# Kernel tuning notes

Hardware: AMD Instinct MI355X
Metric: run time of the kernel (lower is better)

## Reference

```python
import jax, jax.numpy as jnp
import numpy as np

N_NODES = 100000
N_EDGES = 1600000
N_GRAPHS = 64
EMB_DIM = 64
DIMS = [6, 16, 32, 64, EMB_DIM]


def setup_inputs() -> dict:
    key = jax.random.key(0)
    ks = jax.random.split(key, 16)
    feat = jax.random.normal(ks[0], (N_NODES, DIMS[0]), dtype=jnp.float32)
    src = jax.random.randint(ks[1], (N_EDGES,), 0, N_NODES)
    dst = jax.random.randint(ks[2], (N_EDGES,), 0, N_NODES)
    graph_ids = jnp.sort(jax.random.randint(ks[3], (N_NODES,), 0, N_GRAPHS))
    inp = {"feat": feat, "src": src, "dst": dst, "graph_ids": graph_ids}
    # fc_neigh weights for each SAGEConv (gcn aggregator has no fc_self), Xavier-ish init
    for i in range(4):
        din, dout = DIMS[i], DIMS[i + 1]
        scale = 1.0 / np.sqrt(din)
        inp[f"W{i+1}"] = jax.random.uniform(ks[4 + 2 * i], (din, dout), jnp.float32, -scale, scale)
        inp[f"b{i+1}"] = jnp.zeros((dout,), jnp.float32)
    return inp


def _sage_gcn(feat, src, dst, deg, W, b):
    # DGL SAGEConv aggregator_type='gcn':
    # h_neigh = (sum_{u in N(v)} h_u + h_v) / (in_deg(v) + 1); out = h_neigh @ W + b
    neigh = jax.ops.segment_sum(feat[src], dst, num_segments=N_NODES)  # [N, din]
    h = (neigh + feat) / (deg[:, None] + 1.0)
    return h @ W + b


def reference(feat, src, dst, graph_ids, W1, b1, W2, b2, W3, b3, W4, b4):
    deg = jax.ops.segment_sum(jnp.ones((N_EDGES,), feat.dtype), dst, num_segments=N_NODES)
    h = feat
    for W, b in ((W1, b1), (W2, b2), (W3, b3), (W4, b4)):
        h = jax.nn.relu(_sage_gcn(h, src, dst, deg, W, b))
    # dgl.mean_nodes: per-graph mean over nodes
    sums = jax.ops.segment_sum(h, graph_ids, num_segments=N_GRAPHS)          # [G, emb]
    cnts = jax.ops.segment_sum(jnp.ones((N_NODES,), h.dtype), graph_ids, num_segments=N_GRAPHS)
    return sums / jnp.maximum(cnts, 1.0)[:, None]
```

## Files before the change

kernel.cpp:

```cpp
#include <hip/hip_runtime.h>
#include <hip/hip_bf16.h>
#include <hip/hip_fp16.h>

#define N_NODES 100000
#define N_EDGES 1600000
#define N_GRAPHS 64

#define NB_BKT 256
#define NPBKT 391
#define EPB 2048
#define NBLK_BIN ((N_EDGES + EPB - 1) / EPB)


__device__ __forceinline__ __half2 u2h(unsigned int u) {
    return __builtin_bit_cast(__half2, u);
}
__device__ __forceinline__ float2 u2f2(unsigned int u) {
    return __half22float2(u2h(u));
}
__device__ __forceinline__ unsigned int packh2(float a, float b) {
    return __builtin_bit_cast(unsigned int, __float22half2_rn(make_float2(a, b)));
}


__global__ __launch_bounds__(256) void bin_count(const int* __restrict__ dst,
                                                 int* __restrict__ cntmat, int E) {
    __shared__ int cnt[NB_BKT];
    int t = threadIdx.x;
    int e0 = blockIdx.x * EPB;
    cnt[t] = 0;
    __syncthreads();
#pragma unroll
    for (int k = 0; k < 8; ++k) {
        int e = e0 + k * 256 + t;
        if (e < E) {
            unsigned d = (unsigned)dst[e];
            atomicAdd(&cnt[d / (unsigned)NPBKT], 1);
        }
    }
    __syncthreads();
    cntmat[(size_t)blockIdx.x * NB_BKT + t] = cnt[t];
}

__global__ __launch_bounds__(256) void bin_scan(int* __restrict__ cntmat,
                                                int* __restrict__ gcnt, int nblk) {
    __shared__ int s[256];
    int b = blockIdx.x, t = threadIdx.x;
    int running = 0;
    for (int c0 = 0; c0 < nblk; c0 += 256) {
        int idx = c0 + t;
        int v = (idx < nblk) ? cntmat[(size_t)idx * NB_BKT + b] : 0;
        s[t] = v;
        __syncthreads();
        for (int o = 1; o < 256; o <<= 1) {
            int a = (t >= o) ? s[t - o] : 0;
            __syncthreads();
            s[t] += a;
            __syncthreads();
        }
        if (idx < nblk) cntmat[(size_t)idx * NB_BKT + b] = running + s[t] - v;
        running += s[255];
        __syncthreads();
    }
    if (t == 0) gcnt[b] = running;
}

__global__ __launch_bounds__(256) void bin_write(const int* __restrict__ dst,
                                                 const int* __restrict__ src,
                                                 const int* __restrict__ cntmat,
                                                 const int* __restrict__ gcnt,
                                                 uint2* __restrict__ rec, int E) {
    __shared__ int cnt[NB_BKT];
    __shared__ int lbase[NB_BKT];
    __shared__ int gofs[NB_BKT];
    __shared__ uint2 stage[EPB];
    int t = threadIdx.x;
    int e0 = blockIdx.x * EPB;
    int g = gcnt[t];
    lbase[t] = g;
    __syncthreads();
    for (int o = 1; o < 256; o <<= 1) {
        int a = (t >= o) ? lbase[t - o] : 0;
        __syncthreads();
        lbase[t] += a;
        __syncthreads();
    }
    gofs[t] = (lbase[t] - g) + cntmat[(size_t)blockIdx.x * NB_BKT + t];
    cnt[t] = 0;
    __syncthreads();
    int myb[8], mypos[8];
    unsigned myd[8], mys[8];
#pragma unroll
    for (int k = 0; k < 8; ++k) {
        int e = e0 + k * 256 + t;
        if (e < E) {
            unsigned d = (unsigned)dst[e];
            int b = (int)(d / (unsigned)NPBKT);
            myd[k] = d;
            mys[k] = (unsigned)src[e];
            myb[k] = b;
            mypos[k] = atomicAdd(&cnt[b], 1);
        } else {
            myb[k] = -1;
        }
    }
    __syncthreads();
    int c = cnt[t];
    lbase[t] = c;
    __syncthreads();
    for (int o = 1; o < 256; o <<= 1) {
        int a = (t >= o) ? lbase[t - o] : 0;
        __syncthreads();
        lbase[t] += a;
        __syncthreads();
    }
    lbase[t] = lbase[t] - c;
    __syncthreads();
#pragma unroll
    for (int k = 0; k < 8; ++k)
        if (myb[k] >= 0) stage[lbase[myb[k]] + mypos[k]] = make_uint2(myd[k], mys[k]);
    __syncthreads();
    int total = min(EPB, E - e0);
    for (int i = t; i < total; i += 256) {
        int lo = 0, hi = NB_BKT - 1;
        while (lo < hi) {
            int m = (lo + hi + 1) >> 1;
            if (lbase[m] <= i) lo = m; else hi = m - 1;
        }
        rec[(size_t)gofs[lo] + (i - lbase[lo])] = stage[i];
    }
}

__global__ __launch_bounds__(256) void fill_bucket(const uint2* __restrict__ rec,
                                                   const int* __restrict__ gcnt,
                                                   int* __restrict__ rp,
                                                   int* __restrict__ col, int n) {
    __shared__ int sdeg[512];
    __shared__ int lcur[512];
    __shared__ int sg[256];
    __shared__ int lcol[8192];
    int p = blockIdx.x, t = threadIdx.x;
    int nbase = p * NPBKT;
    int nn = min(NPBKT, n - nbase);
    int g = gcnt[t];
    sg[t] = g;
    __syncthreads();
    for (int o = 1; o < 256; o <<= 1) {
        int a = (t >= o) ? sg[t - o] : 0;
        __syncthreads();
        sg[t] += a;
        __syncthreads();
    }
    int ex = sg[t] - g;
    __syncthreads();
    sg[t] = ex;
    __syncthreads();
    int cbase = sg[p];
    int cnt = gcnt[p];
    sdeg[t] = 0;
    sdeg[t + 256] = 0;
    __syncthreads();
    const uint2* r = rec + cbase;
    for (int i = t; i < cnt; i += 256) atomicAdd(&sdeg[r[i].x - (unsigned)nbase], 1);
    __syncthreads();
    int c0 = sdeg[t], c1 = sdeg[t + 256];
    for (int o = 1; o < 512; o <<= 1) {
        int a = (t >= o) ? sdeg[t - o] : 0;
        int b = (t + 256 >= o) ? sdeg[t + 256 - o] : 0;
        __syncthreads();
        sdeg[t] += a;
        sdeg[t + 256] += b;
        __syncthreads();
    }
    int ex0 = sdeg[t] - c0, ex1 = sdeg[t + 256] - c1;
    lcur[t] = ex0;
    lcur[t + 256] = ex1;
    if (t < nn) rp[nbase + t] = cbase + ex0;
    if (t + 256 < nn) rp[nbase + t + 256] = cbase + ex1;
    if (p == NB_BKT - 1 && t == 0) rp[n] = cbase + cnt;
    __syncthreads();
    for (int i = t; i < cnt; i += 256) {
        uint2 e = r[i];
        int slot = atomicAdd(&lcur[e.x - (unsigned)nbase], 1);
        lcol[slot] = (int)e.y;
    }
    __syncthreads();
    for (int i = t; i < cnt; i += 256) col[cbase + i] = lcol[i];
}


__global__ __launch_bounds__(256) void sage_layer1(const float* __restrict__ feat,
                                                   const int* __restrict__ rp,
                                                   const int* __restrict__ col,
                                                   const float* __restrict__ W,
                                                   const float* __restrict__ bias,
                                                   unsigned int* __restrict__ hout, int n) {
    __shared__ float sW[6 * 16];
    __shared__ float sB[16];
    int tid = threadIdx.x;
    if (tid < 96) sW[tid] = W[tid];
    if (tid < 16) sB[tid] = bias[tid];
    __syncthreads();
    int v = blockIdx.x * 256 + tid;
    if (v >= n) return;
    int r0 = rp[v], r1 = rp[v + 1];
    float acc[6] = {0.f, 0.f, 0.f, 0.f, 0.f, 0.f};
    const float2* f2 = reinterpret_cast<const float2*>(feat);
    int j = r0;
    for (; j + 4 <= r1; j += 4) {
        int u0 = col[j], u1 = col[j + 1], u2 = col[j + 2], u3 = col[j + 3];
        float2 a0 = f2[u0 * 3 + 0], b0 = f2[u0 * 3 + 1], c0 = f2[u0 * 3 + 2];
        float2 a1 = f2[u1 * 3 + 0], b1 = f2[u1 * 3 + 1], c1 = f2[u1 * 3 + 2];
        float2 a2 = f2[u2 * 3 + 0], b2 = f2[u2 * 3 + 1], c2 = f2[u2 * 3 + 2];
        float2 a3 = f2[u3 * 3 + 0], b3 = f2[u3 * 3 + 1], c3 = f2[u3 * 3 + 2];
        acc[0] += (a0.x + a1.x) + (a2.x + a3.x);
        acc[1] += (a0.y + a1.y) + (a2.y + a3.y);
        acc[2] += (b0.x + b1.x) + (b2.x + b3.x);
        acc[3] += (b0.y + b1.y) + (b2.y + b3.y);
        acc[4] += (c0.x + c1.x) + (c2.x + c3.x);
        acc[5] += (c0.y + c1.y) + (c2.y + c3.y);
    }
    for (; j < r1; ++j) {
        int u = col[j];
        float2 a = f2[u * 3 + 0], b = f2[u * 3 + 1], c = f2[u * 3 + 2];
        acc[0] += a.x; acc[1] += a.y;
        acc[2] += b.x; acc[3] += b.y;
        acc[4] += c.x; acc[5] += c.y;
    }
    {
        float2 a = f2[v * 3 + 0], b = f2[v * 3 + 1], c = f2[v * 3 + 2];
        acc[0] += a.x; acc[1] += a.y;
        acc[2] += b.x; acc[3] += b.y;
        acc[4] += c.x; acc[5] += c.y;
    }
    float inv = 1.0f / (float)(r1 - r0 + 1);
#pragma unroll
    for (int k = 0; k < 6; ++k) acc[k] *= inv;
    float outv[16];
#pragma unroll
    for (int o = 0; o < 16; ++o) outv[o] = sB[o];
#pragma unroll
    for (int k = 0; k < 6; ++k) {
#pragma unroll
        for (int o = 0; o < 16; ++o) outv[o] += acc[k] * sW[k * 16 + o];
    }
    unsigned int w[8];
#pragma unroll
    for (int o = 0; o < 16; o += 2)
        w[o / 2] = packh2(fmaxf(outv[o], 0.f), fmaxf(outv[o + 1], 0.f));
    uint4* op = reinterpret_cast<uint4*>(hout + v * 8);
    op[0] = make_uint4(w[0], w[1], w[2], w[3]);
    op[1] = make_uint4(w[4], w[5], w[6], w[7]);
}


template <int DIN, int DOUT>
__global__ __launch_bounds__(256) void sage_f16(const uint4* __restrict__ hin,
                                                const int* __restrict__ rp,
                                                const int* __restrict__ col,
                                                const float* __restrict__ W,
                                                const float* __restrict__ bias,
                                                unsigned int* __restrict__ hout, int n) {
    constexpr int WPN = DIN / 8;
    constexpr int NPB = 256 / WPN;
    constexpr int OPT = DOUT / WPN;
    __shared__ float sW[DIN * DOUT];
    __shared__ float sB[DOUT];
    __shared__ float sH[NPB][DIN + 1];

    int tid = threadIdx.x;
    for (int i = tid; i < DIN * DOUT; i += 256) sW[i] = W[i];
    if (tid < DOUT) sB[tid] = bias[tid];

    int sub = tid / WPN;
    int t = tid % WPN;
    int v = blockIdx.x * NPB + sub;

    if (v < n) {
        int r0 = rp[v], r1 = rp[v + 1];
        const __half2 z = __float2half2_rn(0.f);
        __half2 acc[4][4];
#pragma unroll
        for (int s = 0; s < 4; ++s)
#pragma unroll
            for (int q = 0; q < 4; ++q) acc[s][q] = z;
        int j = r0;
        for (; j + 8 <= r1; j += 8) {
            uint4 w[8];
#pragma unroll
            for (int k = 0; k < 8; ++k) w[k] = hin[col[j + k] * WPN + t];
#pragma unroll
            for (int k = 0; k < 8; ++k) {
                __half2* a = acc[k & 3];
                a[0] = __hadd2(a[0], u2h(w[k].x));
                a[1] = __hadd2(a[1], u2h(w[k].y));
                a[2] = __hadd2(a[2], u2h(w[k].z));
                a[3] = __hadd2(a[3], u2h(w[k].w));
            }
        }
        for (; j + 4 <= r1; j += 4) {
            uint4 w[4];
#pragma unroll
            for (int k = 0; k < 4; ++k) w[k] = hin[col[j + k] * WPN + t];
#pragma unroll
            for (int k = 0; k < 4; ++k) {
                __half2* a = acc[k];
                a[0] = __hadd2(a[0], u2h(w[k].x));
                a[1] = __hadd2(a[1], u2h(w[k].y));
                a[2] = __hadd2(a[2], u2h(w[k].z));
                a[3] = __hadd2(a[3], u2h(w[k].w));
            }
        }
        for (; j < r1; ++j) {
            uint4 w = hin[col[j] * WPN + t];
            acc[0][0] = __hadd2(acc[0][0], u2h(w.x));
            acc[0][1] = __hadd2(acc[0][1], u2h(w.y));
            acc[0][2] = __hadd2(acc[0][2], u2h(w.z));
            acc[0][3] = __hadd2(acc[0][3], u2h(w.w));
        }
#pragma unroll
        for (int q = 0; q < 4; ++q)
            acc[0][q] = __hadd2(__hadd2(acc[0][q], acc[1][q]),
                                __hadd2(acc[2][q], acc[3][q]));
        uint4 ws = hin[v * WPN + t];
        unsigned swd[4] = {ws.x, ws.y, ws.z, ws.w};
        float inv = 1.0f / (float)(r1 - r0 + 1);
#pragma unroll
        for (int q = 0; q < 4; ++q) {
            float2 f = __half22float2(acc[0][q]);
            float2 s = u2f2(swd[q]);
            sH[sub][t * 8 + 2 * q + 0] = (f.x + s.x) * inv;
            sH[sub][t * 8 + 2 * q + 1] = (f.y + s.y) * inv;
        }
    }
    __syncthreads();
    if (v < n) {
        int o0 = t * OPT;
        float accO[OPT];
#pragma unroll
        for (int i = 0; i < OPT; ++i) accO[i] = sB[o0 + i];
#pragma unroll 4
        for (int k = 0; k < DIN; ++k) {
            float hk = sH[sub][k];
#pragma unroll
            for (int i = 0; i < OPT; ++i) accO[i] += hk * sW[k * DOUT + o0 + i];
        }
        unsigned wds[OPT / 2];
#pragma unroll
        for (int i = 0; i < OPT; i += 2)
            wds[i / 2] = packh2(fmaxf(accO[i], 0.f), fmaxf(accO[i + 1], 0.f));
        unsigned* op = hout + v * (DOUT / 2) + o0 / 2;
        if constexpr (OPT / 2 == 4) {
            *reinterpret_cast<uint4*>(op) = make_uint4(wds[0], wds[1], wds[2], wds[3]);
        } else if constexpr (OPT / 2 == 8) {
            reinterpret_cast<uint4*>(op)[0] = make_uint4(wds[0], wds[1], wds[2], wds[3]);
            reinterpret_cast<uint4*>(op)[1] = make_uint4(wds[4], wds[5], wds[6], wds[7]);
        } else {
            *reinterpret_cast<uint2*>(op) = make_uint2(wds[0], wds[1]);
        }
    }
}


__device__ __forceinline__ int lower_bound_i(const int* __restrict__ a, int n, int key) {
    int lo = 0, hi = n;
    while (lo < hi) {
        int m = (lo + hi) >> 1;
        if (a[m] < key) lo = m + 1; else hi = m;
    }
    return lo;
}

__global__ __launch_bounds__(256) void pool_f16(const unsigned int* __restrict__ h32,
                                                const int* __restrict__ gids,
                                                float* __restrict__ out, int n) {
    int bx = blockIdx.x;
    int g = bx >> 3, s = bx & 7;
    int start = lower_bound_i(gids, n, g);
    int end = lower_bound_i(gids, n, g + 1);
    int len = end - start;
    float inv = 1.0f / (float)(len > 0 ? len : 1);
    int chunk = (len + 7) / 8;
    int s0 = start + s * chunk;
    int s1 = min(s0 + chunk, end);
    int t = threadIdx.x;
    int d = t & 31, j = t >> 5;
    float a0 = 0.f, a1 = 0.f;
    for (int i = s0 + j; i < s1; i += 8) {
        float2 f = u2f2(h32[(size_t)i * 32 + d]);
        a0 += f.x;
        a1 += f.y;
    }
    __shared__ float red[8][32][2];
    red[j][d][0] = a0;
    red[j][d][1] = a1;
    __syncthreads();
    if (t < 64) {
        int dd = t & 31, e = t >> 5;
        float tot = 0.f;
#pragma unroll
        for (int k = 0; k < 8; ++k) tot += red[k][dd][e];
        atomicAdd(&out[g * 64 + 2 * dd + e], tot * inv);
    }
}


extern "C" void kernel_launch(void* const* d_in, const int* in_sizes, int n_in,
                              void* d_out, int out_size, void* d_ws, size_t ws_size,
                              hipStream_t stream) {
    const int N = N_NODES, E = N_EDGES;
    const float* feat = (const float*)d_in[0];
    const int* src = (const int*)d_in[1];
    const int* dst = (const int*)d_in[2];
    const int* gids = (const int*)d_in[3];
    const float* W1 = (const float*)d_in[4];
    const float* b1 = (const float*)d_in[5];
    const float* W2 = (const float*)d_in[6];
    const float* b2 = (const float*)d_in[7];
    const float* W3 = (const float*)d_in[8];
    const float* b3 = (const float*)d_in[9];
    const float* W4 = (const float*)d_in[10];
    const float* b4 = (const float*)d_in[11];
    float* out = (float*)d_out;

    int* rp = (int*)d_ws;
    int* gcnt = rp + (N + 1);
    int* cntmat = gcnt + 256;
    int* col = cntmat + (size_t)NBLK_BIN * 256;
    size_t off = (size_t)((char*)(col + E) - (char*)d_ws);
    off = (off + 255) & ~(size_t)255;
    unsigned int* h1 = (unsigned int*)((char*)d_ws + off);
    unsigned int* h2 = h1 + (size_t)N * 8;
    unsigned int* h3 = h2 + (size_t)N * 16;
    unsigned int* h4 = h3 + (size_t)N * 32;
    uint2* rec = (uint2*)h3;

    hipMemsetAsync(out, 0, (size_t)N_GRAPHS * 64 * sizeof(float), stream);

    bin_count<<<NBLK_BIN, 256, 0, stream>>>(dst, cntmat, E);
    bin_scan<<<NB_BKT, 256, 0, stream>>>(cntmat, gcnt, NBLK_BIN);
    bin_write<<<NBLK_BIN, 256, 0, stream>>>(dst, src, cntmat, gcnt, rec, E);
    fill_bucket<<<NB_BKT, 256, 0, stream>>>(rec, gcnt, rp, col, N);

    sage_layer1<<<(N + 255) / 256, 256, 0, stream>>>(feat, rp, col, W1, b1, h1, N);
    sage_f16<16, 32><<<(N + 127) / 128, 256, 0, stream>>>(
        (const uint4*)h1, rp, col, W2, b2, h2, N);
    sage_f16<32, 64><<<(N + 63) / 64, 256, 0, stream>>>(
        (const uint4*)h2, rp, col, W3, b3, h3, N);
    sage_f16<64, 64><<<(N + 31) / 32, 256, 0, stream>>>(
        (const uint4*)h3, rp, col, W4, b4, h4, N);

    pool_f16<<<N_GRAPHS * 8, 256, 0, stream>>>(h4, gids, out, N);
}
```

Baseline: 176.8 us.

## Pad CSR rows to multiples of eight with dummy zero node and software-pipeline gathers

Each node's neighbor list is padded to a multiple of eight entries. The padding slots point to a dummy node N whose feature rows are zeroed by memsets, and a separate degree array keeps the true counts. The f16 aggregation loop becomes a branch-free double-buffered loop that issues vectorized int4 index loads and eight gathers ahead of the accumulation. This removes tail loops and overlaps memory latency. The cost is extra padded gather traffic, a larger col buffer, and more LDS in fill_bucket (12288 ints), which assumes the per-bucket padded edge count fits.

```diff
diff --git a/kernel.cpp b/kernel.cpp
--- a/kernel.cpp
+++ b/kernel.cpp
@@ -10,6 +10,7 @@
 #define NPBKT 391
 #define EPB 2048
 #define NBLK_BIN ((N_EDGES + EPB - 1) / EPB)
+#define BKT_SLACK 2744
 
 
 __device__ __forceinline__ __half2 u2h(unsigned int u) {
@@ -134,11 +135,13 @@
 __global__ __launch_bounds__(256) void fill_bucket(const uint2* __restrict__ rec,
                                                    const int* __restrict__ gcnt,
                                                    int* __restrict__ rp,
+                                                   int* __restrict__ deg_out,
                                                    int* __restrict__ col, int n) {
     __shared__ int sdeg[512];
+    __shared__ int pofs[512];
     __shared__ int lcur[512];
     __shared__ int sg[256];
-    __shared__ int lcol[8192];
+    __shared__ int lcol[12288];
     int p = blockIdx.x, t = threadIdx.x;
     int nbase = p * NPBKT;
     int nn = min(NPBKT, n - nbase);
@@ -151,33 +154,40 @@
         sg[t] += a;
         __syncthreads();
     }
-    int ex = sg[t] - g;
-    __syncthreads();
-    sg[t] = ex;
-    __syncthreads();
-    int cbase = sg[p];
+    int exg = sg[t] - g;
+    __syncthreads();
+    sg[t] = exg;
+    __syncthreads();
+    int rbase = sg[p];
     int cnt = gcnt[p];
+    int cbase = ((rbase + 7) & ~7) + p * BKT_SLACK;
     sdeg[t] = 0;
     sdeg[t + 256] = 0;
     __syncthreads();
-    const uint2* r = rec + cbase;
+    const uint2* r = rec + rbase;
     for (int i = t; i < cnt; i += 256) atomicAdd(&sdeg[r[i].x - (unsigned)nbase], 1);
     __syncthreads();
-    int c0 = sdeg[t], c1 = sdeg[t + 256];
+    int d0 = sdeg[t], d1 = sdeg[t + 256];
+    int q0 = (d0 + 7) & ~7, q1 = (d1 + 7) & ~7;
+    pofs[t] = q0;
+    pofs[t + 256] = q1;
+    __syncthreads();
     for (int o = 1; o < 512; o <<= 1) {
-        int a = (t >= o) ? sdeg[t - o] : 0;
-        int b = (t + 256 >= o) ? sdeg[t + 256 - o] : 0;
-        __syncthreads();
-        sdeg[t] += a;
-        sdeg[t + 256] += b;
-        __syncthreads();
-    }
-    int ex0 = sdeg[t] - c0, ex1 = sdeg[t + 256] - c1;
+        int a = (t >= o) ? pofs[t - o] : 0;
+        int b = (t + 256 >= o) ? pofs[t + 256 - o] : 0;
+        __syncthreads();
+        pofs[t] += a;
+        pofs[t + 256] += b;
+        __syncthreads();
+    }
+    int ex0 = pofs[t] - q0, ex1 = pofs[t + 256] - q1;
+    int ptotal = pofs[511];
     lcur[t] = ex0;
     lcur[t + 256] = ex1;
-    if (t < nn) rp[nbase + t] = cbase + ex0;
-    if (t + 256 < nn) rp[nbase + t + 256] = cbase + ex1;
-    if (p == NB_BKT - 1 && t == 0) rp[n] = cbase + cnt;
+    if (t < nn) { rp[nbase + t] = cbase + ex0; deg_out[nbase + t] = d0; }
+    if (t + 256 < nn) { rp[nbase + t + 256] = cbase + ex1; deg_out[nbase + t + 256] = d1; }
+    if (p == NB_BKT - 1 && t == 0) rp[n] = cbase + ptotal;
+    for (int i = t; i < ptotal; i += 256) lcol[i] = n;
     __syncthreads();
     for (int i = t; i < cnt; i += 256) {
         uint2 e = r[i];
@@ -185,12 +195,13 @@
         lcol[slot] = (int)e.y;
     }
     __syncthreads();
-    for (int i = t; i < cnt; i += 256) col[cbase + i] = lcol[i];
+    for (int i = t; i < ptotal; i += 256) col[cbase + i] = lcol[i];
 }
 
 
 __global__ __launch_bounds__(256) void sage_layer1(const float* __restrict__ feat,
                                                    const int* __restrict__ rp,
+                                                   const int* __restrict__ deg,
                                                    const int* __restrict__ col,
                                                    const float* __restrict__ W,
                                                    const float* __restrict__ bias,
@@ -203,7 +214,9 @@
     __syncthreads();
     int v = blockIdx.x * 256 + tid;
     if (v >= n) return;
-    int r0 = rp[v], r1 = rp[v + 1];
+    int r0 = rp[v];
+    int dg = deg[v];
+    int r1 = r0 + dg;
     float acc[6] = {0.f, 0.f, 0.f, 0.f, 0.f, 0.f};
     const float2* f2 = reinterpret_cast<const float2*>(feat);
     int j = r0;
@@ -233,7 +246,7 @@
         acc[2] += b.x; acc[3] += b.y;
         acc[4] += c.x; acc[5] += c.y;
     }
-    float inv = 1.0f / (float)(r1 - r0 + 1);
+    float inv = 1.0f / (float)(dg + 1);
 #pragma unroll
     for (int k = 0; k < 6; ++k) acc[k] *= inv;
     float outv[16];
@@ -257,6 +270,7 @@
 template <int DIN, int DOUT>
 __global__ __launch_bounds__(256) void sage_f16(const uint4* __restrict__ hin,
                                                 const int* __restrict__ rp,
+                                                const int* __restrict__ deg,
                                                 const int* __restrict__ col,
                                                 const float* __restrict__ W,
                                                 const float* __restrict__ bias,
@@ -277,57 +291,63 @@
     int v = blockIdx.x * NPB + sub;
 
     if (v < n) {
-        int r0 = rp[v], r1 = rp[v + 1];
+        int r0 = rp[v];
+        int dg = deg[v];
+        int nb = (dg + 7) >> 3;
         const __half2 z = __float2half2_rn(0.f);
-        __half2 acc[4][4];
-#pragma unroll
-        for (int s = 0; s < 4; ++s)
-#pragma unroll
-            for (int q = 0; q < 4; ++q) acc[s][q] = z;
-        int j = r0;
-        for (; j + 8 <= r1; j += 8) {
-            uint4 w[8];
-#pragma unroll
-            for (int k = 0; k < 8; ++k) w[k] = hin[col[j + k] * WPN + t];
+        __half2 accA[4] = {z, z, z, z}, accB[4] = {z, z, z, z};
+        uint4 wA[8], wB[8];
+
+        auto issue8 = [&](int jj, uint4* w) {
+            int4 cA = *reinterpret_cast<const int4*>(col + jj);
+            int4 cB = *reinterpret_cast<const int4*>(col + jj + 4);
+            w[0] = hin[cA.x * WPN + t];
+            w[1] = hin[cA.y * WPN + t];
+            w[2] = hin[cA.z * WPN + t];
+            w[3] = hin[cA.w * WPN + t];
+            w[4] = hin[cB.x * WPN + t];
+            w[5] = hin[cB.y * WPN + t];
+            w[6] = hin[cB.z * WPN + t];
+            w[7] = hin[cB.w * WPN + t];
+        };
+        auto acc8 = [&](const uint4* w, __half2* a) {
 #pragma unroll
             for (int k = 0; k < 8; ++k) {
-                __half2* a = acc[k & 3];
                 a[0] = __hadd2(a[0], u2h(w[k].x));
                 a[1] = __hadd2(a[1], u2h(w[k].y));
                 a[2] = __hadd2(a[2], u2h(w[k].z));
                 a[3] = __hadd2(a[3], u2h(w[k].w));
             }
-        }
-        for (; j + 4 <= r1; j += 4) {
-            uint4 w[4];
-#pragma unroll
-            for (int k = 0; k < 4; ++k) w[k] = hin[col[j + k] * WPN + t];
-#pragma unroll
-            for (int k = 0; k < 4; ++k) {
-                __half2* a = acc[k];
-                a[0] = __hadd2(a[0], u2h(w[k].x));
-                a[1] = __hadd2(a[1], u2h(w[k].y));
-                a[2] = __hadd2(a[2], u2h(w[k].z));
-                a[3] = __hadd2(a[3], u2h(w[k].w));
+        };
+
+        int j = r0;
+        if (nb > 0) {
+            issue8(j, wA);
+            j += 8;
+            int remaining = nb - 1;
+            while (remaining >= 2) {
+                issue8(j, wB); j += 8;
+                acc8(wA, accA);
+                issue8(j, wA); j += 8;
+                acc8(wB, accB);
+                remaining -= 2;
             }
-        }
-        for (; j < r1; ++j) {
-            uint4 w = hin[col[j] * WPN + t];
-            acc[0][0] = __hadd2(acc[0][0], u2h(w.x));
-            acc[0][1] = __hadd2(acc[0][1], u2h(w.y));
-            acc[0][2] = __hadd2(acc[0][2], u2h(w.z));
-            acc[0][3] = __hadd2(acc[0][3], u2h(w.w));
-        }
-#pragma unroll
-        for (int q = 0; q < 4; ++q)
-            acc[0][q] = __hadd2(__hadd2(acc[0][q], acc[1][q]),
-                                __hadd2(acc[2][q], acc[3][q]));
+            if (remaining == 1) {
+                issue8(j, wB);
+                acc8(wA, accA);
+                acc8(wB, accB);
+            } else {
+                acc8(wA, accA);
+            }
+        }
+#pragma unroll
+        for (int q = 0; q < 4; ++q) accA[q] = __hadd2(accA[q], accB[q]);
         uint4 ws = hin[v * WPN + t];
         unsigned swd[4] = {ws.x, ws.y, ws.z, ws.w};
-        float inv = 1.0f / (float)(r1 - r0 + 1);
+        float inv = 1.0f / (float)(dg + 1);
 #pragma unroll
         for (int q = 0; q < 4; ++q) {
-            float2 f = __half22float2(acc[0][q]);
+            float2 f = __half22float2(accA[q]);
             float2 s = u2f2(swd[q]);
             sH[sub][t * 8 + 2 * q + 0] = (f.x + s.x) * inv;
             sH[sub][t * 8 + 2 * q + 1] = (f.y + s.y) * inv;
@@ -424,31 +444,36 @@
     float* out = (float*)d_out;
 
     int* rp = (int*)d_ws;
-    int* gcnt = rp + (N + 1);
+    int* deg = rp + (N + 1);
+    int* gcnt = deg + N;
     int* cntmat = gcnt + 256;
     int* col = cntmat + (size_t)NBLK_BIN * 256;
-    size_t off = (size_t)((char*)(col + E) - (char*)d_ws);
+    size_t colsz = (size_t)(((E + 7) & ~7) + NB_BKT * BKT_SLACK + 8);
+    size_t off = (size_t)((char*)(col + colsz) - (char*)d_ws);
     off = (off + 255) & ~(size_t)255;
     unsigned int* h1 = (unsigned int*)((char*)d_ws + off);
-    unsigned int* h2 = h1 + (size_t)N * 8;
-    unsigned int* h3 = h2 + (size_t)N * 16;
-    unsigned int* h4 = h3 + (size_t)N * 32;
+    unsigned int* h2 = h1 + (size_t)(N + 1) * 8;
+    unsigned int* h3 = h2 + (size_t)(N + 1) * 16;
+    unsigned int* h4 = h3 + (size_t)(N + 1) * 32;
     uint2* rec = (uint2*)h3;
 
     hipMemsetAsync(out, 0, (size_t)N_GRAPHS * 64 * sizeof(float), stream);
+    hipMemsetAsync(h1 + (size_t)N * 8, 0, 8 * sizeof(unsigned), stream);
+    hipMemsetAsync(h2 + (size_t)N * 16, 0, 16 * sizeof(unsigned), stream);
+    hipMemsetAsync(h3 + (size_t)N * 32, 0, 32 * sizeof(unsigned), stream);
 
     bin_count<<<NBLK_BIN, 256, 0, stream>>>(dst, cntmat, E);
     bin_scan<<<NB_BKT, 256, 0, stream>>>(cntmat, gcnt, NBLK_BIN);
     bin_write<<<NBLK_BIN, 256, 0, stream>>>(dst, src, cntmat, gcnt, rec, E);
-    fill_bucket<<<NB_BKT, 256, 0, stream>>>(rec, gcnt, rp, col, N);
-
-    sage_layer1<<<(N + 255) / 256, 256, 0, stream>>>(feat, rp, col, W1, b1, h1, N);
+    fill_bucket<<<NB_BKT, 256, 0, stream>>>(rec, gcnt, rp, deg, col, N);
+
+    sage_layer1<<<(N + 255) / 256, 256, 0, stream>>>(feat, rp, deg, col, W1, b1, h1, N);
     sage_f16<16, 32><<<(N + 127) / 128, 256, 0, stream>>>(
-        (const uint4*)h1, rp, col, W2, b2, h2, N);
+        (const uint4*)h1, rp, deg, col, W2, b2, h2, N);
     sage_f16<32, 64><<<(N + 63) / 64, 256, 0, stream>>>(
-        (const uint4*)h2, rp, col, W3, b3, h3, N);
+        (const uint4*)h2, rp, deg, col, W3, b3, h3, N);
     sage_f16<64, 64><<<(N + 31) / 32, 256, 0, stream>>>(
-        (const uint4*)h3, rp, col, W4, b4, h4, N);
+        (const uint4*)h3, rp, deg, col, W4, b4, h4, N);
 
     pool_f16<<<N_GRAPHS * 8, 256, 0, stream>>>(h4, gids, out, N);
 }
```

Result: slower. 193.7 us (+9.6%).
